# Performance work log

Hardware: AMD Instinct MI355X
Metric: run time of the kernel (lower is better)

## Reference

```python
import jax, jax.numpy as jnp
import numpy as np

B, D_IN, N, K, L, D_OUT = 64, 1024, 50000, 32, 3, 256


def setup_inputs() -> dict:
    key = jax.random.key(0)
    k = jax.random.split(key, 7)
    x = jax.random.normal(k[0], (B, D_IN), dtype=jnp.float32)
    W0 = jax.random.normal(k[1], (N, D_IN), dtype=jnp.float32) * 0.02
    b0 = jax.random.normal(k[2], (N,), dtype=jnp.float32) * 0.02
    Wv = jax.random.normal(k[3], (L, N, K), dtype=jnp.float32) * 0.1
    Wout = jax.random.normal(k[4], (D_OUT, N), dtype=jnp.float32) * 0.02
    bout = jax.random.normal(k[5], (D_OUT,), dtype=jnp.float32) * 0.02
    src = jax.random.randint(k[6], (L, N, K), 0, N, dtype=jnp.int64)
    return {"x": x, "W0": W0, "b0": b0, "Wv": Wv, "Wout": Wout, "bout": bout, "src": src}


def reference(x, W0, b0, Wv, Wout, bout, src):
    # layer 0: dense input->sources, relu, transpose -> [N, B]
    h = jax.nn.relu(x @ W0.T + b0).T

    # each hidden layer: per-vertex gather of K source activations + 1xK matmul + relu
    def step(h_prev, layer):
        w, s = layer                      # w: [N, K], s: [N, K]
        gathered = h_prev[s]              # [N, K, B] irregular gather
        h_new = jax.nn.relu(jnp.einsum('nk,nkb->nb', w, gathered))
        return h_new, None

    h, _ = jax.lax.scan(step, h, (Wv, src))

    # last layer -> output Linear (the module's _linear_dummy)
    return h.T @ Wout.T + bout            # [B, D_OUT]
```

## Files before the change

kernel.cpp:

```cpp
#include <hip/hip_runtime.h>

#define NV 50000
#define BDIM 64
#define DIN 1024
#define KFAN 32
#define DOUT 256
#define KSTEPS (DIN / 32)

typedef short bf16x8 __attribute__((ext_vector_type(8)));
typedef float f32x4 __attribute__((ext_vector_type(4)));

__device__ __forceinline__ unsigned short bf16_rtn(float f) {
  unsigned u = __float_as_uint(f);
  return (unsigned short)((u + 0x7fffu + ((u >> 16) & 1u)) >> 16);
}
__device__ __forceinline__ float bf16_to_f(unsigned short v) {
  return __uint_as_float(((unsigned)v) << 16);
}

__global__ __launch_bounds__(256) void pack_x(const float* __restrict__ x,
                                              uint4* __restrict__ xpk) {
  int tid = blockIdx.x * 256 + threadIdx.x;
  int ks = tid >> 8;
  int g = (tid >> 6) & 3;
  int l = tid & 63;
  int b = g * 16 + (l & 15);
  int k0 = ks * 32 + (l >> 4) * 8;
  unsigned hi[8], lo[8];
#pragma unroll
  for (int j = 0; j < 8; ++j) {
    float f = x[b * DIN + k0 + j];
    unsigned u = __float_as_uint(f);
    hi[j] = u >> 16;
    float fh = __uint_as_float(u & 0xffff0000u);
    lo[j] = bf16_rtn(f - fh);
  }
  uint4 vh, vl;
  vh.x = hi[0] | (hi[1] << 16); vh.y = hi[2] | (hi[3] << 16);
  vh.z = hi[4] | (hi[5] << 16); vh.w = hi[6] | (hi[7] << 16);
  vl.x = lo[0] | (lo[1] << 16); vl.y = lo[2] | (lo[3] << 16);
  vl.z = lo[4] | (lo[5] << 16); vl.w = lo[6] | (lo[7] << 16);
  xpk[(ks * 4 + g) * 128 + l] = vh;
  xpk[(ks * 4 + g) * 128 + 64 + l] = vl;
}

__global__ __launch_bounds__(64) void layer0_mfma(
    const float* __restrict__ W0, const float* __restrict__ b0,
    const uint4* __restrict__ xpk, unsigned short* __restrict__ h)
{
  const int lane = threadIdx.x;
  const int n_base = blockIdx.x * 32;
  const int rq = lane >> 4;
  const int rr = lane & 15;

  int r0 = n_base + rr;       if (r0 > NV - 1) r0 = NV - 1;
  int r1 = n_base + 16 + rr;  if (r1 > NV - 1) r1 = NV - 1;
  const float* wp0 = W0 + (size_t)r0 * DIN + rq * 8;
  const float* wp1 = W0 + (size_t)r1 * DIN + rq * 8;

  f32x4 acc[2][4];
#pragma unroll
  for (int f = 0; f < 2; ++f)
#pragma unroll
    for (int g = 0; g < 4; ++g) acc[f][g] = (f32x4){0.f, 0.f, 0.f, 0.f};

  float4 wc[2][2];
  uint4 xc[4][2];
  wc[0][0] = *(const float4*)(wp0);
  wc[0][1] = *(const float4*)(wp0 + 4);
  wc[1][0] = *(const float4*)(wp1);
  wc[1][1] = *(const float4*)(wp1 + 4);
#pragma unroll
  for (int g = 0; g < 4; ++g) {
    xc[g][0] = xpk[g * 128 + lane];
    xc[g][1] = xpk[g * 128 + 64 + lane];
  }

  for (int ks = 0; ks < KSTEPS; ++ks) {
    float4 wn[2][2];
    uint4 xn[4][2];
    if (ks + 1 < KSTEPS) {
      const int ko = (ks + 1) * 32;
      wn[0][0] = *(const float4*)(wp0 + ko);
      wn[0][1] = *(const float4*)(wp0 + ko + 4);
      wn[1][0] = *(const float4*)(wp1 + ko);
      wn[1][1] = *(const float4*)(wp1 + ko + 4);
      const int xb = (ks + 1) * 512;
#pragma unroll
      for (int g = 0; g < 4; ++g) {
        xn[g][0] = xpk[xb + g * 128 + lane];
        xn[g][1] = xpk[xb + g * 128 + 64 + lane];
      }
    }
    bf16x8 whi[2], wlo[2];
#pragma unroll
    for (int f = 0; f < 2; ++f) {
      float wf[8] = {wc[f][0].x, wc[f][0].y, wc[f][0].z, wc[f][0].w,
                     wc[f][1].x, wc[f][1].y, wc[f][1].z, wc[f][1].w};
#pragma unroll
      for (int e = 0; e < 8; ++e) {
        unsigned u = __float_as_uint(wf[e]);
        whi[f][e] = (short)(u >> 16);
        float l = wf[e] - __uint_as_float(u & 0xffff0000u);
        wlo[f][e] = (short)bf16_rtn(l);
      }
    }
    bf16x8 xh[4], xl[4];
#pragma unroll
    for (int g = 0; g < 4; ++g) {
      xh[g] = __builtin_bit_cast(bf16x8, xc[g][0]);
      xl[g] = __builtin_bit_cast(bf16x8, xc[g][1]);
    }
#pragma unroll
    for (int f = 0; f < 2; ++f)
#pragma unroll
      for (int g = 0; g < 4; ++g) {
        acc[f][g] = __builtin_amdgcn_mfma_f32_16x16x32_bf16(whi[f], xh[g], acc[f][g], 0, 0, 0);
        acc[f][g] = __builtin_amdgcn_mfma_f32_16x16x32_bf16(wlo[f], xh[g], acc[f][g], 0, 0, 0);
        acc[f][g] = __builtin_amdgcn_mfma_f32_16x16x32_bf16(whi[f], xl[g], acc[f][g], 0, 0, 0);
      }
    if (ks + 1 < KSTEPS) {
#pragma unroll
      for (int f = 0; f < 2; ++f) { wc[f][0] = wn[f][0]; wc[f][1] = wn[f][1]; }
#pragma unroll
      for (int g = 0; g < 4; ++g) { xc[g][0] = xn[g][0]; xc[g][1] = xn[g][1]; }
    }
  }

#pragma unroll
  for (int f = 0; f < 2; ++f)
#pragma unroll
    for (int r = 0; r < 4; ++r) {
      int n = n_base + f * 16 + rq * 4 + r;
      if (n < NV) {
        float bias = b0[n];
#pragma unroll
        for (int g = 0; g < 4; ++g) {
          float v = fmaxf(acc[f][g][r] + bias, 0.f);
          h[(size_t)n * BDIM + g * 16 + rr] = bf16_rtn(v);
        }
      }
    }
}

template <int OUTF32>
__global__ __launch_bounds__(256) void sparse_layer(
    const unsigned short* __restrict__ hin, const float* __restrict__ wv,
    const int* __restrict__ src, void* __restrict__ hout_)
{
  const int lane = threadIdx.x & 63;
  int n = blockIdx.x * 4 + (threadIdx.x >> 6);
  n = __builtin_amdgcn_readfirstlane(n);
  const float* wrow = wv + (size_t)n * KFAN;
  const int* srow = src + (size_t)n * KFAN;
  float acc = 0.f;
#pragma unroll
  for (int k = 0; k < KFAN; ++k) {
    int s = srow[k];
    float w = wrow[k];
    acc = fmaf(w, bf16_to_f(hin[(size_t)s * BDIM + lane]), acc);
  }
  acc = fmaxf(acc, 0.f);
  if (OUTF32)
    ((float*)hout_)[(size_t)n * BDIM + lane] = acc;
  else
    ((unsigned short*)hout_)[(size_t)n * BDIM + lane] = bf16_rtn(acc);
}

constexpr int OC_NC = 256;
constexpr int OC_CHUNKS = (NV + OC_NC - 1) / OC_NC;

__global__ __launch_bounds__(256) void out_partial(
    const float* __restrict__ h, const float* __restrict__ Wout,
    float* __restrict__ part)
{
  __shared__ float hs[64][65];
  __shared__ float wts[64][65];
  const int t = threadIdx.x;
  const int d0 = blockIdx.x * 64;
  const int n0 = blockIdx.y * OC_NC;
  const int tx = t & 15;
  const int ty = t >> 4;
  float acc[4][4] = {};

  for (int ns = 0; ns < OC_NC; ns += 64) {
    const int nb = n0 + ns;
#pragma unroll
    for (int rep = 0; rep < 4; ++rep) {
      int idx = rep * 256 + t;
      int row = idx >> 4;
      int c4 = (idx & 15) * 4;
      int nn = nb + row;
      float4 hv = make_float4(0.f, 0.f, 0.f, 0.f);
      if (nn < NV) hv = *(const float4*)(h + (size_t)nn * BDIM + c4);
      hs[row][c4 + 0] = hv.x; hs[row][c4 + 1] = hv.y;
      hs[row][c4 + 2] = hv.z; hs[row][c4 + 3] = hv.w;
      float4 wv = make_float4(0.f, 0.f, 0.f, 0.f);
      int nc = nb + c4;
      if (nc < NV) wv = *(const float4*)(Wout + (size_t)(d0 + row) * NV + nc);
      wts[c4 + 0][row] = wv.x; wts[c4 + 1][row] = wv.y;
      wts[c4 + 2][row] = wv.z; wts[c4 + 3][row] = wv.w;
    }
    __syncthreads();
#pragma unroll 8
    for (int nn = 0; nn < 64; ++nn) {
      float hb[4], wd[4];
#pragma unroll
      for (int i = 0; i < 4; ++i) hb[i] = hs[nn][tx * 4 + i];
#pragma unroll
      for (int j = 0; j < 4; ++j) wd[j] = wts[nn][ty * 4 + j];
#pragma unroll
      for (int j = 0; j < 4; ++j)
#pragma unroll
        for (int i = 0; i < 4; ++i)
          acc[j][i] = fmaf(wd[j], hb[i], acc[j][i]);
    }
    __syncthreads();
  }
  float* pbase = part + ((size_t)blockIdx.x * OC_CHUNKS + blockIdx.y) * (64 * 64);
#pragma unroll
  for (int j = 0; j < 4; ++j) {
    float4 o = make_float4(acc[j][0], acc[j][1], acc[j][2], acc[j][3]);
    *(float4*)(pbase + (ty * 4 + j) * 64 + tx * 4) = o;
  }
}

__global__ __launch_bounds__(256) void out_reduce(
    const float* __restrict__ part, const float* __restrict__ bout,
    float* __restrict__ out)
{
  int tid = blockIdx.x * 256 + threadIdx.x;
  int b = tid & 63;
  int d = tid >> 6;
  int dtile = d >> 6;
  int dd = d & 63;
  float s = bout[d];
  for (int c = 0; c < OC_CHUNKS; ++c)
    s += part[((size_t)dtile * OC_CHUNKS + c) * 4096 + dd * 64 + b];
  out[(size_t)b * DOUT + d] = s;
}

extern "C" void kernel_launch(void* const* d_in, const int* in_sizes, int n_in,
                              void* d_out, int out_size, void* d_ws, size_t ws_size,
                              hipStream_t stream)
{
  const float* x    = (const float*)d_in[0];
  const float* W0   = (const float*)d_in[1];
  const float* b0   = (const float*)d_in[2];
  const float* Wv   = (const float*)d_in[3];
  const float* Wout = (const float*)d_in[4];
  const float* bout = (const float*)d_in[5];
  const int*   src  = (const int*)d_in[6];
  float* out = (float*)d_out;

  char* ws = (char*)d_ws;
  const size_t hbf_bytes = (size_t)NV * BDIM * 2;
  unsigned short* hb0 = (unsigned short*)ws;
  unsigned short* hb1 = (unsigned short*)(ws + hbf_bytes);
  float* hf = (float*)(ws + 2 * hbf_bytes);
  uint4* xpk  = (uint4*)(ws + 2 * hbf_bytes + (size_t)NV * BDIM * 4);
  float* part = (float*)(ws + 2 * hbf_bytes + (size_t)NV * BDIM * 4);

  pack_x<<<32, 256, 0, stream>>>(x, xpk);
  layer0_mfma<<<(NV + 31) / 32, 64, 0, stream>>>(W0, b0, xpk, hb0);

  const size_t lstride = (size_t)NV * KFAN;
  sparse_layer<0><<<NV / 4, 256, 0, stream>>>(hb0, Wv, src, hb1);
  sparse_layer<0><<<NV / 4, 256, 0, stream>>>(hb1, Wv + lstride, src + lstride, hb0);
  sparse_layer<1><<<NV / 4, 256, 0, stream>>>(hb0, Wv + 2 * lstride, src + 2 * lstride, hf);

  out_partial<<<dim3(4, OC_CHUNKS), 256, 0, stream>>>(hf, Wout, part);
  out_reduce<<<(BDIM * DOUT) / 256, 256, 0, stream>>>(part, bout, out);
}
```

Before: 204.1 us.

## Use split-bf16 MFMA for output GEMM and split gather lanes across K halves

The output projection moves from an FP32 LDS-tiled SIMT GEMM to bf16 MFMA, with Wout split into hi/lo bf16 parts. The last sparse layer now writes bf16 activations in a transposed, padded layout, so the final layer's output is no longer FP32. The sparse gather kernels split each vertex across two blocks of 32 batch columns, with the two wave halves handling alternate K indices and combined by a shuffle. The aim is to cut FP32 FMA cost in the output stage and raise gather parallelism, at the price of bf16 rounding of the last activations and twice as many gather blocks.

```diff
diff --git a/kernel.cpp b/kernel.cpp
--- a/kernel.cpp
+++ b/kernel.cpp
@@ -1,11 +1,14 @@
 #include <hip/hip_runtime.h>
 
 #define NV 50000
+#define NVP 50176
 #define BDIM 64
 #define DIN 1024
 #define KFAN 32
 #define DOUT 256
 #define KSTEPS (DIN / 32)
+#define OPC_CHUNK 128
+#define OPC_NCH (NVP / OPC_CHUNK)
 
 typedef short bf16x8 __attribute__((ext_vector_type(8)));
 typedef float f32x4 __attribute__((ext_vector_type(4)));
@@ -42,6 +45,13 @@
   vl.z = lo[4] | (lo[5] << 16); vl.w = lo[6] | (lo[7] << 16);
   xpk[(ks * 4 + g) * 128 + l] = vh;
   xpk[(ks * 4 + g) * 128 + 64 + l] = vl;
+}
+
+__global__ __launch_bounds__(256) void fill_hT_pad(unsigned short* __restrict__ hT) {
+  int idx = blockIdx.x * 256 + threadIdx.x;
+  int b = idx / (NVP - NV);
+  int n = NV + idx % (NVP - NV);
+  hT[(size_t)b * NVP + n] = 0;
 }
 
 __global__ __launch_bounds__(64) void layer0_mfma(
@@ -143,86 +153,93 @@
     }
 }
 
-template <int OUTF32>
-__global__ __launch_bounds__(256) void sparse_layer(
+template <int LAST>
+__global__ __launch_bounds__(256) void sparse_gather(
     const unsigned short* __restrict__ hin, const float* __restrict__ wv,
-    const int* __restrict__ src, void* __restrict__ hout_)
-{
-  const int lane = threadIdx.x & 63;
-  int n = blockIdx.x * 4 + (threadIdx.x >> 6);
+    const int* __restrict__ src, unsigned short* __restrict__ hout)
+{
+  const int tid = threadIdx.x;
+  const int lane = tid & 63;
+  const int lo = lane & 31;
+  const int khalf = lane >> 5;
+  const int bid = blockIdx.x;
+  const int half = bid & 1;
+  int n = (bid >> 1) * 4 + (tid >> 6);
   n = __builtin_amdgcn_readfirstlane(n);
   const float* wrow = wv + (size_t)n * KFAN;
   const int* srow = src + (size_t)n * KFAN;
   float acc = 0.f;
 #pragma unroll
-  for (int k = 0; k < KFAN; ++k) {
-    int s = srow[k];
-    float w = wrow[k];
-    acc = fmaf(w, bf16_to_f(hin[(size_t)s * BDIM + lane]), acc);
-  }
+  for (int k = 0; k < KFAN; k += 2) {
+    int s0 = srow[k], s1 = srow[k + 1];
+    float w0 = wrow[k], w1 = wrow[k + 1];
+    int s = khalf ? s1 : s0;
+    float w = khalf ? w1 : w0;
+    acc = fmaf(w, bf16_to_f(hin[(size_t)s * BDIM + half * 32 + lo]), acc);
+  }
+  acc += __shfl_xor(acc, 32, 64);
   acc = fmaxf(acc, 0.f);
-  if (OUTF32)
-    ((float*)hout_)[(size_t)n * BDIM + lane] = acc;
-  else
-    ((unsigned short*)hout_)[(size_t)n * BDIM + lane] = bf16_rtn(acc);
-}
-
-constexpr int OC_NC = 256;
-constexpr int OC_CHUNKS = (NV + OC_NC - 1) / OC_NC;
-
-__global__ __launch_bounds__(256) void out_partial(
-    const float* __restrict__ h, const float* __restrict__ Wout,
+  if (khalf == 0) {
+    if (LAST)
+      hout[(size_t)(half * 32 + lo) * NVP + n] = bf16_rtn(acc);
+    else
+      hout[(size_t)n * BDIM + half * 32 + lo] = bf16_rtn(acc);
+  }
+}
+
+__global__ __launch_bounds__(64) void out_partial_mfma(
+    const unsigned short* __restrict__ hT, const float* __restrict__ Wout,
     float* __restrict__ part)
 {
-  __shared__ float hs[64][65];
-  __shared__ float wts[64][65];
-  const int t = threadIdx.x;
-  const int d0 = blockIdx.x * 64;
-  const int n0 = blockIdx.y * OC_NC;
-  const int tx = t & 15;
-  const int ty = t >> 4;
-  float acc[4][4] = {};
-
-  for (int ns = 0; ns < OC_NC; ns += 64) {
-    const int nb = n0 + ns;
-#pragma unroll
-    for (int rep = 0; rep < 4; ++rep) {
-      int idx = rep * 256 + t;
-      int row = idx >> 4;
-      int c4 = (idx & 15) * 4;
-      int nn = nb + row;
-      float4 hv = make_float4(0.f, 0.f, 0.f, 0.f);
-      if (nn < NV) hv = *(const float4*)(h + (size_t)nn * BDIM + c4);
-      hs[row][c4 + 0] = hv.x; hs[row][c4 + 1] = hv.y;
-      hs[row][c4 + 2] = hv.z; hs[row][c4 + 3] = hv.w;
-      float4 wv = make_float4(0.f, 0.f, 0.f, 0.f);
-      int nc = nb + c4;
-      if (nc < NV) wv = *(const float4*)(Wout + (size_t)(d0 + row) * NV + nc);
-      wts[c4 + 0][row] = wv.x; wts[c4 + 1][row] = wv.y;
-      wts[c4 + 2][row] = wv.z; wts[c4 + 3][row] = wv.w;
-    }
-    __syncthreads();
-#pragma unroll 8
-    for (int nn = 0; nn < 64; ++nn) {
-      float hb[4], wd[4];
-#pragma unroll
-      for (int i = 0; i < 4; ++i) hb[i] = hs[nn][tx * 4 + i];
-#pragma unroll
-      for (int j = 0; j < 4; ++j) wd[j] = wts[nn][ty * 4 + j];
-#pragma unroll
-      for (int j = 0; j < 4; ++j)
-#pragma unroll
-        for (int i = 0; i < 4; ++i)
-          acc[j][i] = fmaf(wd[j], hb[i], acc[j][i]);
-    }
-    __syncthreads();
-  }
-  float* pbase = part + ((size_t)blockIdx.x * OC_CHUNKS + blockIdx.y) * (64 * 64);
-#pragma unroll
-  for (int j = 0; j < 4; ++j) {
-    float4 o = make_float4(acc[j][0], acc[j][1], acc[j][2], acc[j][3]);
-    *(float4*)(pbase + (ty * 4 + j) * 64 + tx * 4) = o;
-  }
+  const int lane = threadIdx.x;
+  const int rq = lane >> 4;
+  const int rr = lane & 15;
+  const int dtile = blockIdx.x;
+  const int chunk = blockIdx.y;
+
+  f32x4 acc[4][4];
+#pragma unroll
+  for (int f = 0; f < 4; ++f)
+#pragma unroll
+    for (int g = 0; g < 4; ++g) acc[f][g] = (f32x4){0.f, 0.f, 0.f, 0.f};
+
+#pragma unroll
+  for (int ks = 0; ks < OPC_CHUNK / 32; ++ks) {
+    const int n0 = chunk * OPC_CHUNK + ks * 32 + rq * 8;
+    bf16x8 hb[4];
+#pragma unroll
+    for (int g = 0; g < 4; ++g)
+      hb[g] = *(const bf16x8*)(hT + (size_t)(g * 16 + rr) * NVP + n0);
+    int nb = n0 > (NV - 8) ? (NV - 8) : n0;
+#pragma unroll
+    for (int f = 0; f < 4; ++f) {
+      const float* wp = Wout + (size_t)(dtile * 64 + f * 16 + rr) * NV + nb;
+      float4 a0 = *(const float4*)(wp);
+      float4 a1 = *(const float4*)(wp + 4);
+      float wf[8] = {a0.x, a0.y, a0.z, a0.w, a1.x, a1.y, a1.z, a1.w};
+      bf16x8 whi, wlo;
+#pragma unroll
+      for (int e = 0; e < 8; ++e) {
+        unsigned u = __float_as_uint(wf[e]);
+        whi[e] = (short)(u >> 16);
+        float l = wf[e] - __uint_as_float(u & 0xffff0000u);
+        wlo[e] = (short)bf16_rtn(l);
+      }
+#pragma unroll
+      for (int g = 0; g < 4; ++g) {
+        acc[f][g] = __builtin_amdgcn_mfma_f32_16x16x32_bf16(whi, hb[g], acc[f][g], 0, 0, 0);
+        acc[f][g] = __builtin_amdgcn_mfma_f32_16x16x32_bf16(wlo, hb[g], acc[f][g], 0, 0, 0);
+      }
+    }
+  }
+  float* pbase = part + ((size_t)dtile * OPC_NCH + chunk) * 4096;
+#pragma unroll
+  for (int f = 0; f < 4; ++f)
+#pragma unroll
+    for (int g = 0; g < 4; ++g)
+#pragma unroll
+      for (int r = 0; r < 4; ++r)
+        pbase[(f * 16 + rq * 4 + r) * 64 + g * 16 + rr] = acc[f][g][r];
 }
 
 __global__ __launch_bounds__(256) void out_reduce(
@@ -235,8 +252,8 @@
   int dtile = d >> 6;
   int dd = d & 63;
   float s = bout[d];
-  for (int c = 0; c < OC_CHUNKS; ++c)
-    s += part[((size_t)dtile * OC_CHUNKS + c) * 4096 + dd * 64 + b];
+  for (int c = 0; c < OPC_NCH; ++c)
+    s += part[((size_t)dtile * OPC_NCH + c) * 4096 + dd * 64 + b];
   out[(size_t)b * DOUT + d] = s;
 }
 
@@ -254,21 +271,23 @@
   float* out = (float*)d_out;
 
   char* ws = (char*)d_ws;
-  const size_t hbf_bytes = (size_t)NV * BDIM * 2;
+  const size_t hbf = (size_t)NV * BDIM * 2;
+  const size_t hTb = (size_t)NVP * BDIM * 2;
   unsigned short* hb0 = (unsigned short*)ws;
-  unsigned short* hb1 = (unsigned short*)(ws + hbf_bytes);
-  float* hf = (float*)(ws + 2 * hbf_bytes);
-  uint4* xpk  = (uint4*)(ws + 2 * hbf_bytes + (size_t)NV * BDIM * 4);
-  float* part = (float*)(ws + 2 * hbf_bytes + (size_t)NV * BDIM * 4);
+  unsigned short* hb1 = (unsigned short*)(ws + hbf);
+  unsigned short* hT  = (unsigned short*)(ws + 2 * hbf);
+  uint4* xpk  = (uint4*)(ws + 2 * hbf + hTb);
+  float* part = (float*)(ws + 2 * hbf + hTb + 262144);
 
   pack_x<<<32, 256, 0, stream>>>(x, xpk);
+  fill_hT_pad<<<44, 256, 0, stream>>>(hT);
   layer0_mfma<<<(NV + 31) / 32, 64, 0, stream>>>(W0, b0, xpk, hb0);
 
   const size_t lstride = (size_t)NV * KFAN;
-  sparse_layer<0><<<NV / 4, 256, 0, stream>>>(hb0, Wv, src, hb1);
-  sparse_layer<0><<<NV / 4, 256, 0, stream>>>(hb1, Wv + lstride, src + lstride, hb0);
-  sparse_layer<1><<<NV / 4, 256, 0, stream>>>(hb0, Wv + 2 * lstride, src + 2 * lstride, hf);
-
-  out_partial<<<dim3(4, OC_CHUNKS), 256, 0, stream>>>(hf, Wout, part);
+  sparse_gather<0><<<NV / 2, 256, 0, stream>>>(hb0, Wv, src, hb1);
+  sparse_gather<0><<<NV / 2, 256, 0, stream>>>(hb1, Wv + lstride, src + lstride, hb0);
+  sparse_gather<1><<<NV / 2, 256, 0, stream>>>(hb0, Wv + 2 * lstride, src + 2 * lstride, hT);
+
+  out_partial_mfma<<<dim3(4, OPC_NCH), 64, 0, stream>>>(hT, Wout, part);
   out_reduce<<<(BDIM * DOUT) / 256, 256, 0, stream>>>(part, bout, out);
 }
```

Result: slower. 221.6 us (+8.6%).
